# Kernel optimization log

Measured on AMD Instinct MI355X. Metric: run time of the kernel, lower is better.

The kernel has to match this reference:

```python
import math
import jax, jax.numpy as jnp
import numpy as np

H = 16  # num_heads
B, L, D = 1, 256, 1024


def setup_inputs() -> dict:
    key = jax.random.key(0)
    ks = jax.random.split(key, 12)
    s = 1.0 / math.sqrt(D)  # keep activations O(1)
    inp = {
        "mu": jax.random.normal(ks[0], (B, L, D), jnp.float32),
        "var": jax.random.uniform(ks[1], (B, L, D), jnp.float32) + 0.1,
    }
    names = ["q_mu", "q_var", "k_mu", "k_var", "v_mu", "v_var", "o_mu", "o_var"]
    for i, n in enumerate(names):
        inp["w" + n] = jax.random.normal(ks[2 + i], (D, D), jnp.float32) * s
        inp["b" + n] = jnp.zeros((D,), jnp.float32)
    return inp


def _split_heads(x):
    b, l, d = x.shape
    return x.reshape(b, l, H, d // H).transpose(0, 2, 1, 3)  # [B,H,L,Dh]


def _combine_heads(x):
    b, h, l, dh = x.shape
    return x.transpose(0, 2, 1, 3).reshape(b, l, h * dh)


def reference(mu, var, wq_mu, bq_mu, wq_var, bq_var, wk_mu, bk_mu, wk_var, bk_var,
              wv_mu, bv_mu, wv_var, bv_var, wo_mu, bo_mu, wo_var, bo_var):
    dk = mu.shape[-1] // H
    Qm = _split_heads(mu @ wq_mu + bq_mu)
    Qv = _split_heads(jax.nn.softplus(var @ wq_var + bq_var))
    Km = _split_heads(mu @ wk_mu + bk_mu)
    Kv = _split_heads(jax.nn.softplus(var @ wk_var + bk_var))
    Vm = _split_heads(mu @ wv_mu + bv_mu)
    Vv = _split_heads(jax.nn.softplus(var @ wv_var + bv_var))

    # per-element Gaussian KL, broadcast to [B,H,Lq,Lk,Dh] (as in the original)
    diff = (Qm[:, :, :, None, :] - Km[:, :, None, :, :]) ** 2
    ratio = Qv[:, :, :, None, :] / Kv[:, :, None, :, :]
    kl = diff / (2.0 * Kv[:, :, None, :, :]) + 0.5 * (ratio - jnp.log(ratio) - 1.0)
    scores = -kl.sum(-1) * (1.0 / math.sqrt(dk))  # [B,H,Lq,Lk]
    attn = jax.nn.softmax(scores, axis=-1)

    out_mu = jnp.einsum("bhqk,bhkd->bhqd", attn, Vm)
    out_var = jnp.einsum("bhqk,bhkd->bhqd", attn ** 2, Vv)

    O_mu = _combine_heads(out_mu)
    O_var = _combine_heads(out_var)
    mu_out = O_mu @ wo_mu + bo_mu
    var_out = jax.nn.softplus(O_var @ wo_var + bo_var)
    return mu_out, var_out
```

## Files before the change

### kernel.cpp

```cpp
#include <hip/hip_runtime.h>
#include <math.h>

typedef __bf16 bf16_t;
typedef bf16_t bf16x4 __attribute__((ext_vector_type(4)));
typedef bf16_t bf16x8 __attribute__((ext_vector_type(8)));
typedef float  f32x4  __attribute__((ext_vector_type(4)));

__device__ __forceinline__ float softplus_f(float x) {
    return (x > 20.f) ? x : log1pf(expf(x));
}

__device__ __forceinline__ float fast_rcp(float x) {
#if __has_builtin(__builtin_amdgcn_rcpf)
    return __builtin_amdgcn_rcpf(x);
#else
    return 1.0f / x;
#endif
}

struct PrepArgs { const float* src[8]; const float* mu; const float* var; };

__global__ __launch_bounds__(256) void prep_kernel(PrepArgs pa, bf16_t* __restrict__ wtbase,
                                                   bf16_t* __restrict__ dmu, bf16_t* __restrict__ dvar) {
    const int t = threadIdx.x;
    if (blockIdx.z == 8) {
        const int gid = (blockIdx.y * 16 + blockIdx.x) * 256 + t;
        const float* s; bf16_t* d; int off;
        if (gid < 32768) { s = pa.mu;  d = dmu;  off = gid * 8; }
        else             { s = pa.var; d = dvar; off = (gid - 32768) * 8; }
        float4 v0 = *(const float4*)(s + off);
        float4 v1 = *(const float4*)(s + off + 4);
        bf16x8 o;
        o[0] = (bf16_t)v0.x; o[1] = (bf16_t)v0.y; o[2] = (bf16_t)v0.z; o[3] = (bf16_t)v0.w;
        o[4] = (bf16_t)v1.x; o[5] = (bf16_t)v1.y; o[6] = (bf16_t)v1.z; o[7] = (bf16_t)v1.w;
        *(bf16x8*)(d + off) = o;
        return;
    }
    const int kt = blockIdx.x, nt = blockIdx.y, wm = blockIdx.z;
    const float* __restrict__ W = pa.src[wm];
    bf16_t* __restrict__ Wt = wtbase + (size_t)wm * 1048576;
    __shared__ bf16_t Ts[64][72];
    const int r0 = t >> 4, c4 = (t & 15) * 4;
#pragma unroll
    for (int rep = 0; rep < 4; ++rep) {
        const int r = r0 + rep * 16;
        const float4 v = *(const float4*)&W[(size_t)(kt * 64 + r) * 1024 + nt * 64 + c4];
        Ts[c4 + 0][r] = (bf16_t)v.x;
        Ts[c4 + 1][r] = (bf16_t)v.y;
        Ts[c4 + 2][r] = (bf16_t)v.z;
        Ts[c4 + 3][r] = (bf16_t)v.w;
    }
    __syncthreads();
#pragma unroll
    for (int rep = 0; rep < 2; ++rep) {
        const int chunk = t + rep * 256;
        const int n = chunk >> 3, kc = (chunk & 7) * 8;
        bf16x8 v = *(const bf16x8*)&Ts[n][kc];
        *(bf16x8*)&Wt[(size_t)(nt * 64 + n) * 1024 + kt * 64 + kc] = v;
    }
}

struct GemmArgs {
    const bf16_t* A[6];
    const bf16_t* Wt[6];
    const float*  bias[6];
    float*        dst[6];
    int           splus[6];
};

__global__ __launch_bounds__(256, 2) void gemm_splitk(GemmArgs args) {
    const int z = blockIdx.z;
    const bf16_t* __restrict__ A    = args.A[z];
    const bf16_t* __restrict__ Wt   = args.Wt[z];
    const float*  __restrict__ bias = args.bias[z];
    float*        __restrict__ dst  = args.dst[z];
    const int sp = args.splus[z];

    const int n_base = blockIdx.x * 64;
    const int m_base = blockIdx.y * 64;

    __shared__ __align__(16) unsigned char smem_raw[73728];
    bf16_t* stage = (bf16_t*)smem_raw;
    float*  Cr    = (float*)smem_raw;

    const int t = threadIdx.x;
    const int lane = t & 63;
    const int w = t >> 6;
    bf16_t* As = stage + w * 9216;
    bf16_t* Bs = As + 4608;

    const int r8 = lane >> 3, kb = lane & 7;
    const int fr = lane & 15, fq = lane >> 4, fk = fq * 8;

    const bf16_t* Ab = A  + (size_t)m_base * 1024 + w * 256 + kb * 8;
    const bf16_t* Bb = Wt + (size_t)n_base * 1024 + w * 256 + kb * 8;

    f32x4 acc[4][4] = {};

    bf16x8 pa[8], pb[8];
#pragma unroll
    for (int i = 0; i < 8; ++i) {
        pa[i] = *(const bf16x8*)(Ab + (size_t)(i * 8 + r8) * 1024);
        pb[i] = *(const bf16x8*)(Bb + (size_t)(i * 8 + r8) * 1024);
    }

#pragma unroll
    for (int s = 0; s < 4; ++s) {
#pragma unroll
        for (int i = 0; i < 8; ++i) {
            *(bf16x8*)&As[(i * 8 + r8) * 72 + kb * 8] = pa[i];
            *(bf16x8*)&Bs[(i * 8 + r8) * 72 + kb * 8] = pb[i];
        }
        if (s < 3) {
            const int off = (s + 1) * 64;
#pragma unroll
            for (int i = 0; i < 8; ++i) {
                pa[i] = *(const bf16x8*)(Ab + (size_t)(i * 8 + r8) * 1024 + off);
                pb[i] = *(const bf16x8*)(Bb + (size_t)(i * 8 + r8) * 1024 + off);
            }
        }
#pragma unroll
        for (int kh = 0; kh < 2; ++kh) {
            bf16x8 aF[4], bF[4];
#pragma unroll
            for (int i = 0; i < 4; ++i)
                aF[i] = *(const bf16x8*)&As[(i * 16 + fr) * 72 + kh * 32 + fk];
#pragma unroll
            for (int j = 0; j < 4; ++j)
                bF[j] = *(const bf16x8*)&Bs[(j * 16 + fr) * 72 + kh * 32 + fk];
#pragma unroll
            for (int i = 0; i < 4; ++i)
#pragma unroll
                for (int j = 0; j < 4; ++j)
                    acc[i][j] = __builtin_amdgcn_mfma_f32_16x16x32_bf16(aF[i], bF[j], acc[i][j], 0, 0, 0);
        }
    }

    __syncthreads();
    {
        float* Crw = Cr + w * 4352;
        const int orow = fq * 4;
#pragma unroll
        for (int i = 0; i < 4; ++i)
#pragma unroll
            for (int j = 0; j < 4; ++j)
#pragma unroll
                for (int rr = 0; rr < 4; ++rr)
                    Crw[(i * 16 + orow + rr) * 68 + j * 16 + fr] = acc[i][j][rr];
    }
    __syncthreads();

    const int cc = (t & 15) * 4;
    f32x4 bv4 = *(const f32x4*)&bias[n_base + cc];
#pragma unroll
    for (int i = 0; i < 4; ++i) {
        const int row = (t >> 4) + i * 16;
        f32x4 s0 = *(const f32x4*)&Cr[0 * 4352 + row * 68 + cc];
        f32x4 s1 = *(const f32x4*)&Cr[1 * 4352 + row * 68 + cc];
        f32x4 s2 = *(const f32x4*)&Cr[2 * 4352 + row * 68 + cc];
        f32x4 s3 = *(const f32x4*)&Cr[3 * 4352 + row * 68 + cc];
        f32x4 v = (s0 + s1) + (s2 + s3) + bv4;
        if (sp) {
            v[0] = softplus_f(v[0]); v[1] = softplus_f(v[1]);
            v[2] = softplus_f(v[2]); v[3] = softplus_f(v[3]);
        }
        *(f32x4*)&dst[(size_t)(m_base + row) * 1024 + n_base + cc] = v;
    }
}

__global__ __launch_bounds__(256) void feat_kernel(const float* __restrict__ Km,
                                                   const float* __restrict__ Kv,
                                                   bf16_t* __restrict__ Gbf,
                                                   float* __restrict__ cvec) {
    const int h = blockIdx.x, kb = blockIdx.y;
    const int t = threadIdx.x;
    const int kx = t & 63;
    const int dg = t >> 6;
    const int katt = kb * 64 + kx;
    const float* kvp = Kv + (size_t)katt * 1024 + h * 64 + dg * 16;
    const float* kmp = Km + (size_t)katt * 1024 + h * 64 + dg * 16;
    bf16_t* grow = Gbf + ((size_t)(h * 256 + katt)) * 128;
    float cp = 0.f;
#pragma unroll
    for (int c = 0; c < 4; ++c) {
        f32x4 kv = *(const f32x4*)(kvp + c * 4);
        f32x4 km = *(const f32x4*)(kmp + c * 4);
        bf16x4 o1, o2;
#pragma unroll
        for (int e = 0; e < 4; ++e) {
            const float r = 0.5f * fast_rcp(kv[e]);
            o1[e] = (bf16_t)r;
            o2[e] = (bf16_t)(-2.f * km[e] * r);
            cp += km[e] * km[e] * r + 0.5f * __logf(kv[e]);
        }
        *(bf16x4*)&grow[dg * 16 + c * 4]      = o1;
        *(bf16x4*)&grow[64 + dg * 16 + c * 4] = o2;
    }
    __shared__ float red[4][64];
    red[dg][kx] = cp;
    __syncthreads();
    if (dg == 0)
        cvec[h * 256 + katt] = red[0][kx] + red[1][kx] + red[2][kx] + red[3][kx];
}

#define OFF_VM   0
#define OFF_VV   36864
#define OFF_FS   73728
#define OFF_SC   82176
#define OFF_PHI  98816
#define OFF_PLO  107264
#define OFF_P2H  115712
#define OFF_P2L  124160
#define ATTN_SMEM 132608

__global__ __launch_bounds__(512) void attn_v7(const float* __restrict__ Qm,
                                               const float* __restrict__ Qv,
                                               const bf16_t* __restrict__ Gbf,
                                               const float* __restrict__ cvec,
                                               const float* __restrict__ Vm,
                                               const float* __restrict__ Vv,
                                               bf16_t* __restrict__ Omu,
                                               bf16_t* __restrict__ Ovar) {
    __shared__ __align__(16) unsigned char smem[ATTN_SMEM];
    bf16_t* Vsm = (bf16_t*)(smem + OFF_VM);
    bf16_t* Vsv = (bf16_t*)(smem + OFF_VV);
    float*  Fs  = (float*)(smem + OFF_FS);
    float*  Sc  = (float*)(smem + OFF_SC);
    bf16_t* Phi = (bf16_t*)(smem + OFF_PHI);
    bf16_t* Plo = (bf16_t*)(smem + OFF_PLO);
    bf16_t* P2h = (bf16_t*)(smem + OFF_P2H);
    bf16_t* P2l = (bf16_t*)(smem + OFF_P2L);

    const int qt = blockIdx.x, h = blockIdx.y;
    const int t = threadIdx.x, w = t >> 6, lane = t & 63;
    const int fr = lane & 15, fq = lane >> 4;
    const int n0 = w * 32;

    const bf16_t* gB = Gbf + ((size_t)(h * 256 + n0 + fr)) * 128 + fq * 8;

    bf16x8 bcur[4];
#pragma unroll
    for (int ks = 0; ks < 4; ++ks) bcur[ks] = *(const bf16x8*)(gB + ks * 32);

    if (t < 256) {
        const int r = t >> 4, c = t & 15;
        f32x4 qm = *(const f32x4*)(Qm + (size_t)(qt * 16 + r) * 1024 + h * 64 + c * 4);
        f32x4 qv = *(const f32x4*)(Qv + (size_t)(qt * 16 + r) * 1024 + h * 64 + c * 4);
        *(f32x4*)&Fs[r * 132 + c * 4]      = qm * qm + qv;
        *(f32x4*)&Fs[r * 132 + 64 + c * 4] = qm;
    }
    __syncthreads();

    bf16x8 ahi[4], alo[4];
#pragma unroll
    for (int ks = 0; ks < 4; ++ks) {
        f32x4 f0 = *(const f32x4*)&Fs[fr * 132 + ks * 32 + fq * 8];
        f32x4 f1 = *(const f32x4*)&Fs[fr * 132 + ks * 32 + fq * 8 + 4];
#pragma unroll
        for (int e = 0; e < 4; ++e) {
            bf16_t hb = (bf16_t)f0[e];
            ahi[ks][e] = hb; alo[ks][e] = (bf16_t)(f0[e] - (float)hb);
            bf16_t hb2 = (bf16_t)f1[e];
            ahi[ks][e + 4] = hb2; alo[ks][e + 4] = (bf16_t)(f1[e] - (float)hb2);
        }
    }

    const int tm = t & 255;
    const int vk = tm >> 2, vpart = tm & 3;
    const float* Vsrc = (t >= 256) ? Vv : Vm;
    bf16_t*      Vdst = (t >= 256) ? Vsv : Vsm;

#pragma unroll
    for (int nt = 0; nt < 2; ++nt) {
        const int ra = vk + (2 * nt) * 64;
        const int rb = vk + (2 * nt + 1) * 64;
        const float* vsa = Vsrc + (size_t)ra * 1024 + h * 64 + vpart * 16;
        const float* vsb = Vsrc + (size_t)rb * 1024 + h * 64 + vpart * 16;
        f32x4 va0 = *(const f32x4*)(vsa),     va1 = *(const f32x4*)(vsa + 4);
        f32x4 va2 = *(const f32x4*)(vsa + 8), va3 = *(const f32x4*)(vsa + 12);
        f32x4 vb0 = *(const f32x4*)(vsb),     vb1 = *(const f32x4*)(vsb + 4);
        f32x4 vb2 = *(const f32x4*)(vsb + 8), vb3 = *(const f32x4*)(vsb + 12);

        bf16x8 bnxt[4];
        if (nt < 1) {
#pragma unroll
            for (int ks = 0; ks < 4; ++ks)
                bnxt[ks] = *(const bf16x8*)(gB + 2048 + ks * 32);
        }

        f32x4 acc = {0.f, 0.f, 0.f, 0.f};
#pragma unroll
        for (int ks = 0; ks < 4; ++ks) {
            acc = __builtin_amdgcn_mfma_f32_16x16x32_bf16(ahi[ks], bcur[ks], acc, 0, 0, 0);
            acc = __builtin_amdgcn_mfma_f32_16x16x32_bf16(alo[ks], bcur[ks], acc, 0, 0, 0);
        }

        {
            bf16_t* da = Vdst + ra * 72 + vpart * 16;
            bf16_t* db = Vdst + rb * 72 + vpart * 16;
            bf16x8 o0, o1;
            o0[0]=(bf16_t)va0[0]; o0[1]=(bf16_t)va0[1]; o0[2]=(bf16_t)va0[2]; o0[3]=(bf16_t)va0[3];
            o0[4]=(bf16_t)va1[0]; o0[5]=(bf16_t)va1[1]; o0[6]=(bf16_t)va1[2]; o0[7]=(bf16_t)va1[3];
            o1[0]=(bf16_t)va2[0]; o1[1]=(bf16_t)va2[1]; o1[2]=(bf16_t)va2[2]; o1[3]=(bf16_t)va2[3];
            o1[4]=(bf16_t)va3[0]; o1[5]=(bf16_t)va3[1]; o1[6]=(bf16_t)va3[2]; o1[7]=(bf16_t)va3[3];
            *(bf16x8*)(da)     = o0;
            *(bf16x8*)(da + 8) = o1;
            o0[0]=(bf16_t)vb0[0]; o0[1]=(bf16_t)vb0[1]; o0[2]=(bf16_t)vb0[2]; o0[3]=(bf16_t)vb0[3];
            o0[4]=(bf16_t)vb1[0]; o0[5]=(bf16_t)vb1[1]; o0[6]=(bf16_t)vb1[2]; o0[7]=(bf16_t)vb1[3];
            o1[0]=(bf16_t)vb2[0]; o1[1]=(bf16_t)vb2[1]; o1[2]=(bf16_t)vb2[2]; o1[3]=(bf16_t)vb2[3];
            o1[4]=(bf16_t)vb3[0]; o1[5]=(bf16_t)vb3[1]; o1[6]=(bf16_t)vb3[2]; o1[7]=(bf16_t)vb3[3];
            *(bf16x8*)(db)     = o0;
            *(bf16x8*)(db + 8) = o1;
        }

        const float cv = cvec[h * 256 + n0 + nt * 16 + fr];
        f32x4 lg = (acc + cv) * (-0.125f);
#pragma unroll
        for (int reg = 0; reg < 4; ++reg)
            Sc[(fq * 4 + reg) * 260 + n0 + nt * 16 + fr] = lg[reg];

#pragma unroll
        for (int ks = 0; ks < 4; ++ks) bcur[ks] = bnxt[ks];
    }
    __syncthreads();

    const int fw = w * 2;
    f32x4 sr[2];
#pragma unroll
    for (int r = 0; r < 2; ++r)
        sr[r] = *(const f32x4*)&Sc[(fw + r) * 260 + lane * 4];
#pragma unroll
    for (int r = 0; r < 2; ++r) {
        f32x4 s = sr[r];
        float mloc = fmaxf(fmaxf(s[0], s[1]), fmaxf(s[2], s[3]));
#pragma unroll
        for (int off = 32; off > 0; off >>= 1)
            mloc = fmaxf(mloc, __shfl_xor(mloc, off, 64));
        s[0] = __expf(s[0] - mloc); s[1] = __expf(s[1] - mloc);
        s[2] = __expf(s[2] - mloc); s[3] = __expf(s[3] - mloc);
        float sl = (s[0] + s[1]) + (s[2] + s[3]);
#pragma unroll
        for (int off = 32; off > 0; off >>= 1)
            sl += __shfl_xor(sl, off, 64);
        sr[r] = s * fast_rcp(sl);
    }

#pragma unroll
    for (int r = 0; r < 2; ++r) {
        bf16x4 phi, plo, p2hi, p2lo;
#pragma unroll
        for (int e = 0; e < 4; ++e) {
            const float p = sr[r][e];
            const bf16_t hb = (bf16_t)p;
            phi[e] = hb; plo[e] = (bf16_t)(p - (float)hb);
            const float p2 = p * p;
            const bf16_t h2 = (bf16_t)p2;
            p2hi[e] = h2; p2lo[e] = (bf16_t)(p2 - (float)h2);
        }
        const int row = fw + r;
        *(bf16x4*)&Phi[row * 264 + lane * 4] = phi;
        *(bf16x4*)&Plo[row * 264 + lane * 4] = plo;
        *(bf16x4*)&P2h[row * 264 + lane * 4] = p2hi;
        *(bf16x4*)&P2l[row * 264 + lane * 4] = p2lo;
    }
    __syncthreads();

    const int tile = w & 3;
    const int isvar = w >> 2;
    const bf16_t* Pa = isvar ? P2h : Phi;
    const bf16_t* Pb = isvar ? P2l : Plo;
    const bf16_t* Vs = isvar ? Vsv : Vsm;
    f32x4 accp = {0.f, 0.f, 0.f, 0.f};
#pragma unroll
    for (int k0 = 0; k0 < 256; k0 += 32) {
        const int ka = k0 + fq * 8;
        bf16x8 a1 = *(const bf16x8*)&Pa[fr * 264 + ka];
        bf16x8 a2 = *(const bf16x8*)&Pb[fr * 264 + ka];
        bf16x8 bfr;
#pragma unroll
        for (int j = 0; j < 8; ++j)
            bfr[j] = Vs[(ka + j) * 72 + tile * 16 + fr];
        accp = __builtin_amdgcn_mfma_f32_16x16x32_bf16(a1, bfr, accp, 0, 0, 0);
        accp = __builtin_amdgcn_mfma_f32_16x16x32_bf16(a2, bfr, accp, 0, 0, 0);
    }

    bf16_t* Out = isvar ? Ovar : Omu;
#pragma unroll
    for (int reg = 0; reg < 4; ++reg) {
        const int qg = qt * 16 + fq * 4 + reg;
        const size_t ob = (size_t)qg * 1024 + h * 64 + tile * 16 + fr;
        Out[ob] = (bf16_t)accp[reg];
    }
}

extern "C" void kernel_launch(void* const* d_in, const int* in_sizes, int n_in,
                              void* d_out, int out_size, void* d_ws, size_t ws_size,
                              hipStream_t stream) {
    const float* mu  = (const float*)d_in[0];
    const float* var = (const float*)d_in[1];

    uint8_t* ws = (uint8_t*)d_ws;
    bf16_t* Abf_mu  = (bf16_t*)(ws);
    bf16_t* Abf_var = (bf16_t*)(ws + (512u << 10));
    bf16_t* WtB     = (bf16_t*)(ws + (1u << 20));
    float*  Proj    = (float*)(ws + (17u << 20));
    bf16_t* Obf_mu  = (bf16_t*)(ws + (23u << 20));
    bf16_t* Obf_var = (bf16_t*)(ws + (23u << 20) + (512u << 10));
    bf16_t* Gbf     = (bf16_t*)(ws + (24u << 20));
    float*  cvec    = (float*)(ws + (25u << 20));

    PrepArgs pa;
    for (int i = 0; i < 8; ++i) pa.src[i] = (const float*)d_in[2 + 2 * i];
    pa.mu = mu; pa.var = var;
    prep_kernel<<<dim3(16, 16, 9), 256, 0, stream>>>(pa, WtB, Abf_mu, Abf_var);

    GemmArgs g1;
    for (int z = 0; z < 6; ++z) {
        g1.A[z]    = (z & 1) ? Abf_var : Abf_mu;
        g1.Wt[z]   = WtB + (size_t)z * 1048576;
        g1.bias[z] = (const float*)d_in[3 + 2 * z];
        g1.dst[z]  = Proj + (size_t)z * 262144;
        g1.splus[z] = (z & 1);
    }
    gemm_splitk<<<dim3(16, 4, 6), 256, 0, stream>>>(g1);

    feat_kernel<<<dim3(16, 4), 256, 0, stream>>>(Proj + 2 * 262144, Proj + 3 * 262144, Gbf, cvec);

    attn_v7<<<dim3(16, 16), 512, 0, stream>>>(Proj,
                                              Proj + 262144,
                                              Gbf, cvec,
                                              Proj + 4 * 262144,
                                              Proj + 5 * 262144,
                                              Obf_mu, Obf_var);

    GemmArgs g3;
    for (int z = 0; z < 6; ++z) {
        g3.A[z]    = Obf_mu;
        g3.Wt[z]   = WtB + (size_t)6 * 1048576;
        g3.bias[z] = (const float*)d_in[15];
        g3.dst[z]  = (float*)d_out;
        g3.splus[z] = 0;
    }
    g3.A[1]    = Obf_var;
    g3.Wt[1]   = WtB + (size_t)7 * 1048576;
    g3.bias[1] = (const float*)d_in[17];
    g3.dst[1]  = (float*)d_out + 262144;
    g3.splus[1] = 1;
    gemm_splitk<<<dim3(16, 4, 2), 256, 0, stream>>>(g3);
}
```

Before: 148.9 us.

## Fuse K-feature computation into projection GEMM epilogue, drop feat_kernel launch

The K mean and K variance projections now run back to back inside a single GEMM block, and the epilogue computes the KL feature rows (Gbf) and the per-key constant (cvec) directly. This removes the separate feat_kernel launch and the fp32 write and read of Km and Kv through global memory. In exchange, the fused z-slice blocks do twice the GEMM work serially, so that slice can become the critical path, and the grid drops from 6 to 5 z-slices.

```diff
diff --git a/kernel.cpp b/kernel.cpp
--- a/kernel.cpp
+++ b/kernel.cpp
@@ -60,147 +60,182 @@
     }
 }
 
+__device__ __forceinline__ void gemm_tile64(const bf16_t* __restrict__ A,
+                                            const bf16_t* __restrict__ Wt,
+                                            int m_base, int n_base,
+                                            unsigned char* smem_raw, int t, f32x4 out[4]) {
+    __syncthreads();
+    bf16_t* stage = (bf16_t*)smem_raw;
+    float*  Cr    = (float*)smem_raw;
+
+    const int lane = t & 63;
+    const int w = t >> 6;
+    bf16_t* As = stage + w * 9216;
+    bf16_t* Bs = As + 4608;
+
+    const int r8 = lane >> 3, kb = lane & 7;
+    const int fr = lane & 15, fq = lane >> 4, fk = fq * 8;
+
+    const bf16_t* Ab = A  + (size_t)m_base * 1024 + w * 256 + kb * 8;
+    const bf16_t* Bb = Wt + (size_t)n_base * 1024 + w * 256 + kb * 8;
+
+    f32x4 acc[4][4] = {};
+
+    bf16x8 pa[8], pb[8];
+#pragma unroll
+    for (int i = 0; i < 8; ++i) {
+        pa[i] = *(const bf16x8*)(Ab + (size_t)(i * 8 + r8) * 1024);
+        pb[i] = *(const bf16x8*)(Bb + (size_t)(i * 8 + r8) * 1024);
+    }
+
+#pragma unroll
+    for (int s = 0; s < 4; ++s) {
+#pragma unroll
+        for (int i = 0; i < 8; ++i) {
+            *(bf16x8*)&As[(i * 8 + r8) * 72 + kb * 8] = pa[i];
+            *(bf16x8*)&Bs[(i * 8 + r8) * 72 + kb * 8] = pb[i];
+        }
+        if (s < 3) {
+            const int off = (s + 1) * 64;
+#pragma unroll
+            for (int i = 0; i < 8; ++i) {
+                pa[i] = *(const bf16x8*)(Ab + (size_t)(i * 8 + r8) * 1024 + off);
+                pb[i] = *(const bf16x8*)(Bb + (size_t)(i * 8 + r8) * 1024 + off);
+            }
+        }
+#pragma unroll
+        for (int kh = 0; kh < 2; ++kh) {
+            bf16x8 aF[4], bF[4];
+#pragma unroll
+            for (int i = 0; i < 4; ++i)
+                aF[i] = *(const bf16x8*)&As[(i * 16 + fr) * 72 + kh * 32 + fk];
+#pragma unroll
+            for (int j = 0; j < 4; ++j)
+                bF[j] = *(const bf16x8*)&Bs[(j * 16 + fr) * 72 + kh * 32 + fk];
+#pragma unroll
+            for (int i = 0; i < 4; ++i)
+#pragma unroll
+                for (int j = 0; j < 4; ++j)
+                    acc[i][j] = __builtin_amdgcn_mfma_f32_16x16x32_bf16(aF[i], bF[j], acc[i][j], 0, 0, 0);
+        }
+    }
+
+    __syncthreads();
+    {
+        float* Crw = Cr + w * 4352;
+        const int orow = fq * 4;
+#pragma unroll
+        for (int i = 0; i < 4; ++i)
+#pragma unroll
+            for (int j = 0; j < 4; ++j)
+#pragma unroll
+                for (int rr = 0; rr < 4; ++rr)
+                    Crw[(i * 16 + orow + rr) * 68 + j * 16 + fr] = acc[i][j][rr];
+    }
+    __syncthreads();
+
+    const int cc = (t & 15) * 4;
+#pragma unroll
+    for (int i = 0; i < 4; ++i) {
+        const int row = (t >> 4) + i * 16;
+        f32x4 s0 = *(const f32x4*)&Cr[0 * 4352 + row * 68 + cc];
+        f32x4 s1 = *(const f32x4*)&Cr[1 * 4352 + row * 68 + cc];
+        f32x4 s2 = *(const f32x4*)&Cr[2 * 4352 + row * 68 + cc];
+        f32x4 s3 = *(const f32x4*)&Cr[3 * 4352 + row * 68 + cc];
+        out[i] = (s0 + s1) + (s2 + s3);
+    }
+}
+
 struct GemmArgs {
     const bf16_t* A[6];
     const bf16_t* Wt[6];
     const float*  bias[6];
     float*        dst[6];
     int           splus[6];
+    int           fused[6];
+    const bf16_t* A2[6];
+    const bf16_t* Wt2[6];
+    const float*  bias2[6];
+    bf16_t* Gbf;
+    float*  cvec;
 };
 
 __global__ __launch_bounds__(256, 2) void gemm_splitk(GemmArgs args) {
     const int z = blockIdx.z;
-    const bf16_t* __restrict__ A    = args.A[z];
-    const bf16_t* __restrict__ Wt   = args.Wt[z];
-    const float*  __restrict__ bias = args.bias[z];
-    float*        __restrict__ dst  = args.dst[z];
-    const int sp = args.splus[z];
-
     const int n_base = blockIdx.x * 64;
     const int m_base = blockIdx.y * 64;
 
     __shared__ __align__(16) unsigned char smem_raw[73728];
-    bf16_t* stage = (bf16_t*)smem_raw;
-    float*  Cr    = (float*)smem_raw;
-
     const int t = threadIdx.x;
-    const int lane = t & 63;
-    const int w = t >> 6;
-    bf16_t* As = stage + w * 9216;
-    bf16_t* Bs = As + 4608;
-
-    const int r8 = lane >> 3, kb = lane & 7;
-    const int fr = lane & 15, fq = lane >> 4, fk = fq * 8;
-
-    const bf16_t* Ab = A  + (size_t)m_base * 1024 + w * 256 + kb * 8;
-    const bf16_t* Bb = Wt + (size_t)n_base * 1024 + w * 256 + kb * 8;
-
-    f32x4 acc[4][4] = {};
-
-    bf16x8 pa[8], pb[8];
-#pragma unroll
-    for (int i = 0; i < 8; ++i) {
-        pa[i] = *(const bf16x8*)(Ab + (size_t)(i * 8 + r8) * 1024);
-        pb[i] = *(const bf16x8*)(Bb + (size_t)(i * 8 + r8) * 1024);
-    }
-
-#pragma unroll
-    for (int s = 0; s < 4; ++s) {
-#pragma unroll
-        for (int i = 0; i < 8; ++i) {
-            *(bf16x8*)&As[(i * 8 + r8) * 72 + kb * 8] = pa[i];
-            *(bf16x8*)&Bs[(i * 8 + r8) * 72 + kb * 8] = pb[i];
-        }
-        if (s < 3) {
-            const int off = (s + 1) * 64;
-#pragma unroll
-            for (int i = 0; i < 8; ++i) {
-                pa[i] = *(const bf16x8*)(Ab + (size_t)(i * 8 + r8) * 1024 + off);
-                pb[i] = *(const bf16x8*)(Bb + (size_t)(i * 8 + r8) * 1024 + off);
+    const int cc = (t & 15) * 4;
+
+    if (!args.fused[z]) {
+        f32x4 out[4];
+        gemm_tile64(args.A[z], args.Wt[z], m_base, n_base, smem_raw, t, out);
+        const int sp = args.splus[z];
+        float* __restrict__ dst = args.dst[z];
+        f32x4 bv4 = *(const f32x4*)&args.bias[z][n_base + cc];
+#pragma unroll
+        for (int i = 0; i < 4; ++i) {
+            const int row = (t >> 4) + i * 16;
+            f32x4 v = out[i] + bv4;
+            if (sp) {
+                v[0] = softplus_f(v[0]); v[1] = softplus_f(v[1]);
+                v[2] = softplus_f(v[2]); v[3] = softplus_f(v[3]);
             }
-        }
-#pragma unroll
-        for (int kh = 0; kh < 2; ++kh) {
-            bf16x8 aF[4], bF[4];
-#pragma unroll
-            for (int i = 0; i < 4; ++i)
-                aF[i] = *(const bf16x8*)&As[(i * 16 + fr) * 72 + kh * 32 + fk];
-#pragma unroll
-            for (int j = 0; j < 4; ++j)
-                bF[j] = *(const bf16x8*)&Bs[(j * 16 + fr) * 72 + kh * 32 + fk];
-#pragma unroll
-            for (int i = 0; i < 4; ++i)
-#pragma unroll
-                for (int j = 0; j < 4; ++j)
-                    acc[i][j] = __builtin_amdgcn_mfma_f32_16x16x32_bf16(aF[i], bF[j], acc[i][j], 0, 0, 0);
-        }
-    }
-
-    __syncthreads();
+            *(f32x4*)&dst[(size_t)(m_base + row) * 1024 + n_base + cc] = v;
+        }
+        return;
+    }
+
+    const int h = blockIdx.x;
+    f32x4 km4[4], kv4[4];
     {
-        float* Crw = Cr + w * 4352;
-        const int orow = fq * 4;
-#pragma unroll
-        for (int i = 0; i < 4; ++i)
-#pragma unroll
-            for (int j = 0; j < 4; ++j)
-#pragma unroll
-                for (int rr = 0; rr < 4; ++rr)
-                    Crw[(i * 16 + orow + rr) * 68 + j * 16 + fr] = acc[i][j][rr];
-    }
-    __syncthreads();
-
-    const int cc = (t & 15) * 4;
-    f32x4 bv4 = *(const f32x4*)&bias[n_base + cc];
+        f32x4 out[4];
+        gemm_tile64(args.A[z], args.Wt[z], m_base, n_base, smem_raw, t, out);
+        f32x4 b1 = *(const f32x4*)&args.bias[z][n_base + cc];
+#pragma unroll
+        for (int i = 0; i < 4; ++i) km4[i] = out[i] + b1;
+    }
+    {
+        f32x4 out[4];
+        gemm_tile64(args.A2[z], args.Wt2[z], m_base, n_base, smem_raw, t, out);
+        f32x4 b2 = *(const f32x4*)&args.bias2[z][n_base + cc];
+#pragma unroll
+        for (int i = 0; i < 4; ++i) {
+            f32x4 v = out[i] + b2;
+            kv4[i][0] = softplus_f(v[0]); kv4[i][1] = softplus_f(v[1]);
+            kv4[i][2] = softplus_f(v[2]); kv4[i][3] = softplus_f(v[3]);
+        }
+    }
+    __syncthreads();
+    float* part = (float*)smem_raw;
 #pragma unroll
     for (int i = 0; i < 4; ++i) {
         const int row = (t >> 4) + i * 16;
-        f32x4 s0 = *(const f32x4*)&Cr[0 * 4352 + row * 68 + cc];
-        f32x4 s1 = *(const f32x4*)&Cr[1 * 4352 + row * 68 + cc];
-        f32x4 s2 = *(const f32x4*)&Cr[2 * 4352 + row * 68 + cc];
-        f32x4 s3 = *(const f32x4*)&Cr[3 * 4352 + row * 68 + cc];
-        f32x4 v = (s0 + s1) + (s2 + s3) + bv4;
-        if (sp) {
-            v[0] = softplus_f(v[0]); v[1] = softplus_f(v[1]);
-            v[2] = softplus_f(v[2]); v[3] = softplus_f(v[3]);
-        }
-        *(f32x4*)&dst[(size_t)(m_base + row) * 1024 + n_base + cc] = v;
-    }
-}
-
-__global__ __launch_bounds__(256) void feat_kernel(const float* __restrict__ Km,
-                                                   const float* __restrict__ Kv,
-                                                   bf16_t* __restrict__ Gbf,
-                                                   float* __restrict__ cvec) {
-    const int h = blockIdx.x, kb = blockIdx.y;
-    const int t = threadIdx.x;
-    const int kx = t & 63;
-    const int dg = t >> 6;
-    const int katt = kb * 64 + kx;
-    const float* kvp = Kv + (size_t)katt * 1024 + h * 64 + dg * 16;
-    const float* kmp = Km + (size_t)katt * 1024 + h * 64 + dg * 16;
-    bf16_t* grow = Gbf + ((size_t)(h * 256 + katt)) * 128;
-    float cp = 0.f;
-#pragma unroll
-    for (int c = 0; c < 4; ++c) {
-        f32x4 kv = *(const f32x4*)(kvp + c * 4);
-        f32x4 km = *(const f32x4*)(kmp + c * 4);
         bf16x4 o1, o2;
+        float cp = 0.f;
 #pragma unroll
         for (int e = 0; e < 4; ++e) {
-            const float r = 0.5f * fast_rcp(kv[e]);
+            const float kv = kv4[i][e];
+            const float km = km4[i][e];
+            const float r = 0.5f * fast_rcp(kv);
             o1[e] = (bf16_t)r;
-            o2[e] = (bf16_t)(-2.f * km[e] * r);
-            cp += km[e] * km[e] * r + 0.5f * __logf(kv[e]);
-        }
-        *(bf16x4*)&grow[dg * 16 + c * 4]      = o1;
-        *(bf16x4*)&grow[64 + dg * 16 + c * 4] = o2;
-    }
-    __shared__ float red[4][64];
-    red[dg][kx] = cp;
-    __syncthreads();
-    if (dg == 0)
-        cvec[h * 256 + katt] = red[0][kx] + red[1][kx] + red[2][kx] + red[3][kx];
+            o2[e] = (bf16_t)(-2.f * km * r);
+            cp += km * km * r + 0.5f * __logf(kv);
+        }
+        bf16_t* grow = args.Gbf + ((size_t)(h * 256 + m_base + row)) * 128;
+        *(bf16x4*)&grow[cc]      = o1;
+        *(bf16x4*)&grow[64 + cc] = o2;
+        part[row * 16 + (t & 15)] = cp;
+    }
+    __syncthreads();
+    if (t < 64) {
+        float s = 0.f;
+#pragma unroll
+        for (int j = 0; j < 16; ++j) s += part[t * 16 + j];
+        args.cvec[h * 256 + m_base + t] = s;
+    }
 }
 
 #define OFF_VM   0
@@ -414,17 +449,20 @@
     pa.mu = mu; pa.var = var;
     prep_kernel<<<dim3(16, 16, 9), 256, 0, stream>>>(pa, WtB, Abf_mu, Abf_var);
 
-    GemmArgs g1;
-    for (int z = 0; z < 6; ++z) {
-        g1.A[z]    = (z & 1) ? Abf_var : Abf_mu;
-        g1.Wt[z]   = WtB + (size_t)z * 1048576;
-        g1.bias[z] = (const float*)d_in[3 + 2 * z];
-        g1.dst[z]  = Proj + (size_t)z * 262144;
-        g1.splus[z] = (z & 1);
-    }
-    gemm_splitk<<<dim3(16, 4, 6), 256, 0, stream>>>(g1);
-
-    feat_kernel<<<dim3(16, 4), 256, 0, stream>>>(Proj + 2 * 262144, Proj + 3 * 262144, Gbf, cvec);
+    GemmArgs g1 = {};
+    g1.Gbf = Gbf; g1.cvec = cvec;
+    g1.A[0] = Abf_mu;  g1.Wt[0] = WtB + 0 * 1048576; g1.bias[0] = (const float*)d_in[3];
+    g1.dst[0] = Proj;                 g1.splus[0] = 0; g1.fused[0] = 0;
+    g1.A[1] = Abf_var; g1.Wt[1] = WtB + 1 * 1048576; g1.bias[1] = (const float*)d_in[5];
+    g1.dst[1] = Proj + 262144;        g1.splus[1] = 1; g1.fused[1] = 0;
+    g1.A[2] = Abf_mu;  g1.Wt[2] = WtB + 4 * 1048576; g1.bias[2] = (const float*)d_in[11];
+    g1.dst[2] = Proj + 4 * 262144;    g1.splus[2] = 0; g1.fused[2] = 0;
+    g1.A[3] = Abf_var; g1.Wt[3] = WtB + 5 * 1048576; g1.bias[3] = (const float*)d_in[13];
+    g1.dst[3] = Proj + 5 * 262144;    g1.splus[3] = 1; g1.fused[3] = 0;
+    g1.A[4]  = Abf_mu;  g1.Wt[4]  = WtB + 2 * 1048576; g1.bias[4]  = (const float*)d_in[7];
+    g1.A2[4] = Abf_var; g1.Wt2[4] = WtB + 3 * 1048576; g1.bias2[4] = (const float*)d_in[9];
+    g1.dst[4] = nullptr; g1.splus[4] = 0; g1.fused[4] = 1;
+    gemm_splitk<<<dim3(16, 4, 5), 256, 0, stream>>>(g1);
 
     attn_v7<<<dim3(16, 16), 512, 0, stream>>>(Proj,
                                               Proj + 262144,
@@ -433,18 +471,11 @@
                                               Proj + 5 * 262144,
                                               Obf_mu, Obf_var);
 
-    GemmArgs g3;
-    for (int z = 0; z < 6; ++z) {
-        g3.A[z]    = Obf_mu;
-        g3.Wt[z]   = WtB + (size_t)6 * 1048576;
-        g3.bias[z] = (const float*)d_in[15];
-        g3.dst[z]  = (float*)d_out;
-        g3.splus[z] = 0;
-    }
-    g3.A[1]    = Obf_var;
-    g3.Wt[1]   = WtB + (size_t)7 * 1048576;
-    g3.bias[1] = (const float*)d_in[17];
-    g3.dst[1]  = (float*)d_out + 262144;
-    g3.splus[1] = 1;
+    GemmArgs g3 = {};
+    g3.Gbf = Gbf; g3.cvec = cvec;
+    g3.A[0] = Obf_mu;  g3.Wt[0] = WtB + 6 * 1048576; g3.bias[0] = (const float*)d_in[15];
+    g3.dst[0] = (float*)d_out;            g3.splus[0] = 0; g3.fused[0] = 0;
+    g3.A[1] = Obf_var; g3.Wt[1] = WtB + 7 * 1048576; g3.bias[1] = (const float*)d_in[17];
+    g3.dst[1] = (float*)d_out + 262144;   g3.splus[1] = 1; g3.fused[1] = 0;
     gemm_splitk<<<dim3(16, 4, 2), 256, 0, stream>>>(g3);
 }
```

Result: slower. 153.3 us (+3.0%).
